# Performance work log

Measured on AMD Instinct MI355X. Metric: run time of the kernel, lower is better.

Reference implementation:

```python
import jax, jax.numpy as jnp
import numpy as np

B, T, DIM_IN, DIM_REC, DIM_OUT = 64, 1000, 128, 512, 64
DT, TAU = 1.0, 10.0

def retanh(x):
    return jnp.maximum(jnp.tanh(x), 0.0)

def setup_inputs() -> dict:
    key = jax.random.key(0)
    ks = jax.random.split(key, 8)
    s_rr = 1.0 / np.sqrt(DIM_REC)
    s_xr = 1.0 / np.sqrt(DIM_IN)
    return {
        "input": jax.random.normal(ks[0], (B, T, DIM_IN), jnp.float32),
        "brneverlearn": 0.1 * jax.random.normal(ks[1], (B, T, DIM_REC), jnp.float32),
        "Wrx": jax.random.uniform(ks[2], (DIM_REC, DIM_IN), jnp.float32, -s_xr, s_xr),
        "bx": jax.random.uniform(ks[3], (DIM_REC,), jnp.float32, -s_xr, s_xr),
        "Wrr": jax.random.uniform(ks[4], (DIM_REC, DIM_REC), jnp.float32, -s_rr, s_rr),
        "Wyr": jax.random.uniform(ks[5], (DIM_OUT, DIM_REC), jnp.float32, -s_rr, s_rr),
        "by": jax.random.uniform(ks[6], (DIM_OUT,), jnp.float32, -s_rr, s_rr),
        "r0": jnp.zeros((DIM_REC,), jnp.float32),
    }

def reference(input, brneverlearn, Wrx, bx, Wrr, Wyr, by, r0):
    # Precompute input drive for all timesteps: [B,T,R]
    x_drive = jnp.einsum('bti,ri->btr', input, Wrx) + bx
    a = DT / TAU

    def step(r, inp):
        xd_t, br_t = inp  # [B,R] each
        f = retanh(r @ Wrr.T + xd_t)
        r_new = r + a * (-r + f + br_t)
        return r_new, r_new

    r_init = jnp.broadcast_to(r0, (B, DIM_REC))
    # scan over time: [T,B,R]
    _, rstore_t = jax.lax.scan(step, r_init,
                               (jnp.swapaxes(x_drive, 0, 1),
                                jnp.swapaxes(brneverlearn, 0, 1)))
    rstore = jnp.swapaxes(rstore_t, 0, 1)  # [B,T,R]
    y = jnp.einsum('btr,or->bto', rstore, Wyr) + by
    return (y, rstore)
```

## Files before the change

kernel.cpp:

```cpp
#include <hip/hip_runtime.h>
#include <stdint.h>

#define B_  64
#define T_  1000
#define DI_ 128
#define DR_ 512
#define DO_ 64

static __device__ __forceinline__ float bfu(uint16_t u){
  union{uint32_t i; float f;} v; v.i = ((uint32_t)u) << 16; return v.f;
}
static __device__ __forceinline__ uint16_t f2bf(float f){
  union{float f; uint32_t i;} v; v.f = f;
  uint32_t i = v.i;
  return (uint16_t)((i + 0x7FFFu + ((i >> 16) & 1u)) >> 16);
}

template<int BF16> struct IO;
template<> struct IO<1> {
  static __device__ __forceinline__ float ld(const void* p, size_t i){ return bfu(((const uint16_t*)p)[i]); }
  static __device__ __forceinline__ void  st(void* p, size_t i, float v){ ((uint16_t*)p)[i] = f2bf(v); }
};
template<> struct IO<0> {
  static __device__ __forceinline__ float ld(const void* p, size_t i){ return ((const float*)p)[i]; }
  static __device__ __forceinline__ void  st(void* p, size_t i, float v){ ((float*)p)[i] = v; }
};

static __device__ __forceinline__ float retanh_f(float x){
  if (x <= 0.f) return 0.f;
  float e = __expf(2.f * x);
  return 1.f - 2.f / (e + 1.f);
}

static __device__ __forceinline__ unsigned long long poll_l2_u64(const unsigned long long* p){
  unsigned long long v, z = 0ull;
  asm volatile("global_atomic_or_x2 %0, %1, %2, off sc0\n\t"
               "s_waitcnt vmcnt(0)"
               : "=&v"(v) : "v"(p), "v"(z) : "memory");
  return v;
}

static __device__ __forceinline__ void pub_l2_u64(unsigned long long* p, unsigned long long pkt){
  asm volatile("global_atomic_swap_x2 %0, %1, off"
               :: "v"(p), "v"(pkt) : "memory");
}

__global__ void init_kernel(const uint16_t* __restrict__ bx, int* __restrict__ flag,
                            unsigned long long* __restrict__ rglobA){
  size_t i = (size_t)blockIdx.x * blockDim.x + threadIdx.x;
  const size_t n = (size_t)2 * B_ * DR_;
  if (i < n) { rglobA[i] = 0ull; rglobA[i + n] = 0ull; }
  if (i == 0) {
    int small = 0;
    for (int k = 0; k < 24; ++k) {
      uint16_t u = bx[2 * k];
      uint16_t e = (u >> 7) & 0xFF;
      small += (e <= 124) ? 1 : 0;
    }
    *flag = (small == 24) ? 1 : 0;
  }
}

template<int BF16>
__global__ __launch_bounds__(512)
void rnn_run(const void* __restrict__ inp,
             const void* __restrict__ br,
             const void* __restrict__ Wrx,
             const void* __restrict__ bx,
             const void* __restrict__ Wrr,
             const void* __restrict__ r0,
             void* __restrict__ rstore,
             const int* __restrict__ flag,
             unsigned long long* __restrict__ rglobA,
             unsigned long long* __restrict__ rglobB)
{
  if (*flag != BF16) return;
  const int blk = blockIdx.x;
  const int b   = blk & 63;
  const int s   = blk >> 6;
  const int tid = threadIdx.x;
  const int q   = tid >> 7;
  const int rl  = tid & 127;
  const int row = s * 128 + rl;

  __shared__ __align__(16) float s_r[DR_];
  __shared__ __align__(16) float s_in[DI_];
  __shared__ __align__(16) float s_part[DR_];

  float w[128];
  #pragma unroll
  for (int k = 0; k < 128; ++k)
    w[k] = IO<BF16>::ld(Wrr, (size_t)row * DR_ + q * 128 + k);
  float wx[32];
  #pragma unroll
  for (int k = 0; k < 32; ++k)
    wx[k] = IO<BF16>::ld(Wrx, (size_t)row * DI_ + q * 32 + k);

  const float bxj = (q == 0) ? IO<BF16>::ld(bx, row) : 0.f;
  float rj        = (q == 0) ? IO<BF16>::ld(r0, row) : 0.f;

  s_r[tid & 511] = IO<BF16>::ld(r0, tid & 511);
  if (tid < DI_) s_in[tid] = IO<BF16>::ld(inp, (size_t)b * T_ * DI_ + tid);

  const int j = tid - 128;
  const int g = j + ((j >= s * 128) ? 128 : 0);

  const size_t base_in = (size_t)b * T_ * DI_;
  const size_t base_r  = (size_t)b * T_ * DR_;
  const size_t ex_base = (size_t)b * DR_;
  bool ok = true;
  bool use_fast = true;
  int  strikes  = 0;
  __syncthreads();

  #pragma unroll 1
  for (int t = 0; t < T_; ++t) {
    float brv = 0.f, inv = 0.f;
    if (q == 0) {
      brv = IO<BF16>::ld(br, base_r + (size_t)t * DR_ + row);
      if (t + 1 < T_)
        inv = IO<BF16>::ld(inp, base_in + (size_t)(t + 1) * DI_ + rl);
    }

    float a0 = 0.f, a1 = 0.f, a2 = 0.f, a3 = 0.f;
    const float* rq = s_r + q * 128;
    #pragma unroll
    for (int k = 0; k < 128; k += 4) {
      float4 rv = *(const float4*)(rq + k);
      a0 = fmaf(w[k + 0], rv.x, a0);
      a1 = fmaf(w[k + 1], rv.y, a1);
      a2 = fmaf(w[k + 2], rv.z, a2);
      a3 = fmaf(w[k + 3], rv.w, a3);
    }
    const float* iq = s_in + q * 32;
    #pragma unroll
    for (int k = 0; k < 32; k += 4) {
      float4 iv = *(const float4*)(iq + k);
      a0 = fmaf(wx[k + 0], iv.x, a0);
      a1 = fmaf(wx[k + 1], iv.y, a1);
      a2 = fmaf(wx[k + 2], iv.z, a2);
      a3 = fmaf(wx[k + 3], iv.w, a3);
    }
    s_part[rl * 4 + q] = (a0 + a1) + (a2 + a3);
    __syncthreads();

    const size_t slot = ((size_t)(t & 1) * B_) * DR_;

    if (q == 0) {
      float4 p  = *(const float4*)(s_part + rl * 4);
      float tot = (p.x + p.y) + (p.z + p.w) + bxj;
      float f   = retanh_f(tot);
      rj = rj + 0.1f * (f + brv - rj);
      IO<BF16>::st(rstore, base_r + (size_t)t * DR_ + row, rj);
      s_r[row] = rj;
      if (t + 1 < T_) {
        s_in[rl] = inv;
        union { float f; unsigned u; } cv; cv.f = rj;
        unsigned long long pkt =
            ((unsigned long long)(unsigned)(t + 1) << 32) | (unsigned long long)cv.u;
        pub_l2_u64(&rglobB[slot + ex_base + row], pkt);
        __hip_atomic_store(&rglobA[slot + ex_base + row], pkt,
                           __ATOMIC_RELAXED, __HIP_MEMORY_SCOPE_AGENT);
      }
    } else if (t + 1 < T_) {
      const unsigned want = (unsigned)(t + 1);
      const unsigned long long* aF = &rglobB[slot + ex_base + g];
      const unsigned long long* aS = &rglobA[slot + ex_base + g];
      unsigned long long v = 0;
      bool got = false;
      if (use_fast) {
        int f = 32;
        do {
          v = poll_l2_u64(aF);
          if ((unsigned)(v >> 32) == want) { got = true; strikes = 0; break; }
        } while (--f);
        if (!got && ++strikes >= 2) use_fast = false;
      }
      if (!got) {
        if (ok) {
          int spins = 200000;
          for (;;) {
            v = __hip_atomic_load(aS, __ATOMIC_RELAXED, __HIP_MEMORY_SCOPE_AGENT);
            if ((unsigned)(v >> 32) == want) break;
            __builtin_amdgcn_s_sleep(1);
            if (--spins == 0) { ok = false; break; }
          }
        } else {
          v = __hip_atomic_load(aS, __ATOMIC_RELAXED, __HIP_MEMORY_SCOPE_AGENT);
        }
      }
      union { unsigned u; float f; } cv; cv.u = (unsigned)v;
      s_r[g] = cv.f;
    }
    __syncthreads();
  }
}

template<int BF16>
__global__ __launch_bounds__(256)
void ygemm(const void* __restrict__ Wyr,
           const void* __restrict__ by,
           const void* __restrict__ rstore,
           void* __restrict__ y,
           const int* __restrict__ flag)
{
  if (*flag != BF16) return;
  const int tid  = threadIdx.x;
  const int wave = tid >> 6;
  const int lane = tid & 63;
  const int base = blockIdx.x * 64;

  __shared__ __align__(16) float rs_c[64 * 128];
  __shared__ __align__(16) float wy_c[64 * 132];

  float acc[16];
  #pragma unroll
  for (int i = 0; i < 16; ++i) acc[i] = 0.f;

  #pragma unroll 1
  for (int kc = 0; kc < 4; ++kc) {
    for (int n = tid; n < 8192; n += 256) {
      int r = n >> 7, k = n & 127;
      rs_c[r * 128 + k] = IO<BF16>::ld(rstore, (size_t)(base + r) * DR_ + kc * 128 + k);
    }
    for (int n = tid; n < 8192; n += 256) {
      int o = n >> 7, k = n & 127;
      wy_c[o * 132 + k] = IO<BF16>::ld(Wyr, (size_t)o * DR_ + kc * 128 + k);
    }
    __syncthreads();

    float4 wf[32];
    #pragma unroll
    for (int m = 0; m < 32; ++m)
      wf[m] = *(const float4*)(wy_c + lane * 132 + m * 4);

    #pragma unroll 1
    for (int i = 0; i < 16; ++i) {
      int r = wave * 16 + i;
      float s0 = 0.f, s1 = 0.f, s2 = 0.f, s3 = 0.f;
      #pragma unroll
      for (int m = 0; m < 32; ++m) {
        float4 rv = *(const float4*)(rs_c + r * 128 + m * 4);
        s0 = fmaf(wf[m].x, rv.x, s0);
        s1 = fmaf(wf[m].y, rv.y, s1);
        s2 = fmaf(wf[m].z, rv.z, s2);
        s3 = fmaf(wf[m].w, rv.w, s3);
      }
      acc[i] += (s0 + s1) + (s2 + s3);
    }
    __syncthreads();
  }

  const float byl = IO<BF16>::ld(by, lane);
  #pragma unroll
  for (int i = 0; i < 16; ++i) {
    int r = base + wave * 16 + i;
    IO<BF16>::st(y, (size_t)r * DO_ + lane, acc[i] + byl);
  }
}

extern "C" void kernel_launch(void* const* d_in, const int* in_sizes, int n_in,
                              void* d_out, int out_size, void* d_ws, size_t ws_size,
                              hipStream_t stream) {
  const void* inp = d_in[0];
  const void* brn = d_in[1];
  const void* Wrx = d_in[2];
  const void* bx  = d_in[3];
  const void* Wrr = d_in[4];
  const void* Wyr = d_in[5];
  const void* by  = d_in[6];
  const void* r0  = d_in[7];

  char* ws = (char*)d_ws;
  int*                flag   = (int*)ws;
  unsigned long long* rglobA = (unsigned long long*)(ws + 4096);
  unsigned long long* rglobB = rglobA + (size_t)2 * B_ * DR_;

  uint16_t* y_bf  = (uint16_t*)d_out;
  uint16_t* rs_bf = y_bf + (size_t)B_ * T_ * DO_;
  float*    y_f   = (float*)d_out;
  float*    rs_f  = y_f + (size_t)B_ * T_ * DO_;

  hipLaunchKernelGGL(init_kernel, dim3(512), dim3(256), 0, stream,
                     (const uint16_t*)bx, flag, rglobA);

  hipLaunchKernelGGL((rnn_run<1>), dim3(4 * B_), dim3(512), 0, stream,
                     inp, brn, Wrx, bx, Wrr, r0, (void*)rs_bf, flag, rglobA, rglobB);
  hipLaunchKernelGGL((rnn_run<0>), dim3(4 * B_), dim3(512), 0, stream,
                     inp, brn, Wrx, bx, Wrr, r0, (void*)rs_f, flag, rglobA, rglobB);

  hipLaunchKernelGGL((ygemm<1>), dim3((B_ * T_) / 64), dim3(256), 0, stream,
                     Wyr, by, (const void*)rs_bf, (void*)y_bf, flag);
  hipLaunchKernelGGL((ygemm<0>), dim3((B_ * T_) / 64), dim3(256), 0, stream,
                     Wyr, by, (const void*)rs_f, (void*)y_f, flag);
}
```

Measured before the change: 2.328 ms.

## Probe L2 atomic visibility once at startup and publish on a single channel

After: 2.366 ms. About the same (+1.6%).

```diff
diff --git a/kernel.cpp b/kernel.cpp
--- a/kernel.cpp
+++ b/kernel.cpp
@@ -45,11 +45,22 @@
                :: "v"(p), "v"(pkt) : "memory");
 }
 
+static __device__ __forceinline__ void bar_lds(){
+  asm volatile("s_waitcnt lgkmcnt(0)" ::: "memory");
+  __builtin_amdgcn_sched_barrier(0);
+  __builtin_amdgcn_s_barrier();
+  __builtin_amdgcn_sched_barrier(0);
+}
+
 __global__ void init_kernel(const uint16_t* __restrict__ bx, int* __restrict__ flag,
+                            unsigned* __restrict__ nonce,
+                            unsigned* __restrict__ det,
+                            unsigned long long* __restrict__ probe,
                             unsigned long long* __restrict__ rglobA){
   size_t i = (size_t)blockIdx.x * blockDim.x + threadIdx.x;
   const size_t n = (size_t)2 * B_ * DR_;
   if (i < n) { rglobA[i] = 0ull; rglobA[i + n] = 0ull; }
+  if (i < 256) { det[i] = 0u; probe[i] = 0ull; }
   if (i == 0) {
     int small = 0;
     for (int k = 0; k < 24; ++k) {
@@ -58,6 +69,9 @@
       small += (e <= 124) ? 1 : 0;
     }
     *flag = (small == 24) ? 1 : 0;
+    unsigned long long rt = __builtin_amdgcn_s_memrealtime();
+    __hip_atomic_store(nonce, (((unsigned)(rt >> 4)) & 0x3FFFFFu) | 1u,
+                       __ATOMIC_RELAXED, __HIP_MEMORY_SCOPE_AGENT);
   }
 }
 
@@ -71,6 +85,9 @@
              const void* __restrict__ r0,
              void* __restrict__ rstore,
              const int* __restrict__ flag,
+             const unsigned* __restrict__ nonce_p,
+             unsigned* __restrict__ det,
+             unsigned long long* __restrict__ probe,
              unsigned long long* __restrict__ rglobA,
              unsigned long long* __restrict__ rglobB)
 {
@@ -86,6 +103,8 @@
   __shared__ __align__(16) float s_r[DR_];
   __shared__ __align__(16) float s_in[DI_];
   __shared__ __align__(16) float s_part[DR_];
+  __shared__ unsigned s_nonce;
+  __shared__ int s_fast;
 
   float w[128];
   #pragma unroll
@@ -102,6 +121,36 @@
   s_r[tid & 511] = IO<BF16>::ld(r0, tid & 511);
   if (tid < DI_) s_in[tid] = IO<BF16>::ld(inp, (size_t)b * T_ * DI_ + tid);
 
+  if (tid == 0) {
+    const unsigned nr = __hip_atomic_load(nonce_p, __ATOMIC_RELAXED,
+                                          __HIP_MEMORY_SCOPE_AGENT);
+    const unsigned long long MAGIC =
+        ((unsigned long long)nr << 32) | 0xD00DFEEDull;
+    pub_l2_u64(&probe[b * 4 + s], MAGIC);
+    unsigned got = 0; const unsigned all = 0xFu & ~(1u << s);
+    int w2 = 20000;
+    while (got != all && w2--) {
+      #pragma unroll
+      for (int i = 0; i < 4; ++i)
+        if (i != s && !(got & (1u << i)))
+          if (poll_l2_u64(&probe[b * 4 + i]) == MAGIC) got |= 1u << i;
+    }
+    __hip_atomic_store(&det[b * 4 + s], (got == all) ? 3u : 1u,
+                       __ATOMIC_RELAXED, __HIP_MEMORY_SCOPE_AGENT);
+    unsigned fastv = 1u;
+    for (int i = 0; i < 4; ++i) {
+      unsigned u; long spins = 4000000;
+      while ((u = __hip_atomic_load(&det[b * 4 + i], __ATOMIC_RELAXED,
+                                    __HIP_MEMORY_SCOPE_AGENT)) == 0u) {
+        __builtin_amdgcn_s_sleep(2);
+        if (--spins == 0) { u = 1u; break; }
+      }
+      fastv &= (u == 3u) ? 1u : 0u;
+    }
+    s_fast  = (int)fastv;
+    s_nonce = nr;
+  }
+
   const int j = tid - 128;
   const int g = j + ((j >= s * 128) ? 128 : 0);
 
@@ -109,17 +158,23 @@
   const size_t base_r  = (size_t)b * T_ * DR_;
   const size_t ex_base = (size_t)b * DR_;
   bool ok = true;
-  bool use_fast = true;
-  int  strikes  = 0;
+
+  float brv_c = 0.f, inv_c = 0.f;
+  if (q == 0) {
+    brv_c = IO<BF16>::ld(br, base_r + row);
+    if (T_ > 1) inv_c = IO<BF16>::ld(inp, base_in + DI_ + rl);
+  }
   __syncthreads();
+  const unsigned nonce = s_nonce;
+  const bool     fastp = (s_fast != 0);
 
   #pragma unroll 1
   for (int t = 0; t < T_; ++t) {
-    float brv = 0.f, inv = 0.f;
-    if (q == 0) {
-      brv = IO<BF16>::ld(br, base_r + (size_t)t * DR_ + row);
-      if (t + 1 < T_)
-        inv = IO<BF16>::ld(inp, base_in + (size_t)(t + 1) * DI_ + rl);
+    float brv_n = 0.f, inv_n = 0.f;
+    if (q == 0 && t + 1 < T_) {
+      brv_n = IO<BF16>::ld(br, base_r + (size_t)(t + 1) * DR_ + row);
+      if (t + 2 < T_)
+        inv_n = IO<BF16>::ld(inp, base_in + (size_t)(t + 2) * DI_ + rl);
     }
 
     float a0 = 0.f, a1 = 0.f, a2 = 0.f, a3 = 0.f;
@@ -142,7 +197,7 @@
       a3 = fmaf(wx[k + 3], iv.w, a3);
     }
     s_part[rl * 4 + q] = (a0 + a1) + (a2 + a3);
-    __syncthreads();
+    bar_lds();
 
     const size_t slot = ((size_t)(t & 1) * B_) * DR_;
 
@@ -150,33 +205,40 @@
       float4 p  = *(const float4*)(s_part + rl * 4);
       float tot = (p.x + p.y) + (p.z + p.w) + bxj;
       float f   = retanh_f(tot);
-      rj = rj + 0.1f * (f + brv - rj);
+      rj = rj + 0.1f * (f + brv_c - rj);
+      if (t + 1 < T_) {
+        union { float f; unsigned u; } cv; cv.f = rj;
+        const unsigned tag = (nonce << 10) | (unsigned)(t + 1);
+        unsigned long long pkt =
+            ((unsigned long long)tag << 32) | (unsigned long long)cv.u;
+        if (fastp) {
+          pub_l2_u64(&rglobB[slot + ex_base + row], pkt);
+        } else {
+          __hip_atomic_store(&rglobA[slot + ex_base + row], pkt,
+                             __ATOMIC_RELAXED, __HIP_MEMORY_SCOPE_AGENT);
+        }
+      }
+      s_r[row] = rj;
+      if (t + 1 < T_) s_in[rl] = inv_c;
       IO<BF16>::st(rstore, base_r + (size_t)t * DR_ + row, rj);
-      s_r[row] = rj;
-      if (t + 1 < T_) {
-        s_in[rl] = inv;
-        union { float f; unsigned u; } cv; cv.f = rj;
-        unsigned long long pkt =
-            ((unsigned long long)(unsigned)(t + 1) << 32) | (unsigned long long)cv.u;
-        pub_l2_u64(&rglobB[slot + ex_base + row], pkt);
-        __hip_atomic_store(&rglobA[slot + ex_base + row], pkt,
-                           __ATOMIC_RELAXED, __HIP_MEMORY_SCOPE_AGENT);
-      }
+      brv_c = brv_n; inv_c = inv_n;
     } else if (t + 1 < T_) {
-      const unsigned want = (unsigned)(t + 1);
-      const unsigned long long* aF = &rglobB[slot + ex_base + g];
-      const unsigned long long* aS = &rglobA[slot + ex_base + g];
+      const unsigned want = (nonce << 10) | (unsigned)(t + 1);
       unsigned long long v = 0;
-      bool got = false;
-      if (use_fast) {
-        int f = 32;
-        do {
+      if (fastp) {
+        const unsigned long long* aF = &rglobB[slot + ex_base + g];
+        if (ok) {
+          int spins = 300000;
+          for (;;) {
+            v = poll_l2_u64(aF);
+            if ((unsigned)(v >> 32) == want) break;
+            if (--spins == 0) { ok = false; break; }
+          }
+        } else {
           v = poll_l2_u64(aF);
-          if ((unsigned)(v >> 32) == want) { got = true; strikes = 0; break; }
-        } while (--f);
-        if (!got && ++strikes >= 2) use_fast = false;
-      }
-      if (!got) {
+        }
+      } else {
+        const unsigned long long* aS = &rglobA[slot + ex_base + g];
         if (ok) {
           int spins = 200000;
           for (;;) {
@@ -192,7 +254,7 @@
       union { unsigned u; float f; } cv; cv.u = (unsigned)v;
       s_r[g] = cv.f;
     }
-    __syncthreads();
+    bar_lds();
   }
 }
 
@@ -273,6 +335,9 @@
 
   char* ws = (char*)d_ws;
   int*                flag   = (int*)ws;
+  unsigned*           nonce  = (unsigned*)(ws + 64);
+  unsigned*           det    = (unsigned*)(ws + 256);
+  unsigned long long* probe  = (unsigned long long*)(ws + 2048);
   unsigned long long* rglobA = (unsigned long long*)(ws + 4096);
   unsigned long long* rglobB = rglobA + (size_t)2 * B_ * DR_;
 
@@ -282,12 +347,14 @@
   float*    rs_f  = y_f + (size_t)B_ * T_ * DO_;
 
   hipLaunchKernelGGL(init_kernel, dim3(512), dim3(256), 0, stream,
-                     (const uint16_t*)bx, flag, rglobA);
+                     (const uint16_t*)bx, flag, nonce, det, probe, rglobA);
 
   hipLaunchKernelGGL((rnn_run<1>), dim3(4 * B_), dim3(512), 0, stream,
-                     inp, brn, Wrx, bx, Wrr, r0, (void*)rs_bf, flag, rglobA, rglobB);
+                     inp, brn, Wrx, bx, Wrr, r0, (void*)rs_bf, flag,
+                     nonce, det, probe, rglobA, rglobB);
   hipLaunchKernelGGL((rnn_run<0>), dim3(4 * B_), dim3(512), 0, stream,
-                     inp, brn, Wrx, bx, Wrr, r0, (void*)rs_f, flag, rglobA, rglobB);
+                     inp, brn, Wrx, bx, Wrr, r0, (void*)rs_f, flag,
+                     nonce, det, probe, rglobA, rglobB);
 
   hipLaunchKernelGGL((ygemm<1>), dim3((B_ * T_) / 64), dim3(256), 0, stream,
                      Wyr, by, (const void*)rs_bf, (void*)y_bf, flag);
```
